# Performance work log

Measured on AMD Instinct MI355X. Metric: run time of the kernel, lower is better.

Reference implementation:

```python
import jax, jax.numpy as jnp
import numpy as np

N = 8192      # nodes
E = 262144    # edges (avg degree 32)
NFEAT = 1024
NHID = 512
ZDIM = 32


def _uniform(key, shape, stdv):
    return jax.random.uniform(key, shape, jnp.float32, -stdv, stdv)


def setup_inputs() -> dict:
    key = jax.random.key(0)
    ks = jax.random.split(key, 10)
    x = jax.random.normal(ks[0], (N, NFEAT), jnp.float32)
    adj_rows = jnp.sort(jax.random.randint(ks[1], (E,), 0, N))
    adj_cols = jax.random.randint(ks[2], (E,), 0, N)
    # positive edge weights, roughly row-normalized (avg degree 32)
    adj_vals = jax.random.uniform(ks[3], (E,), jnp.float32) / 32.0
    s0 = 1.0 / np.sqrt(NHID).astype(np.float32)
    s1 = 1.0 / np.sqrt(ZDIM).astype(np.float32)
    W0 = _uniform(ks[4], (NFEAT, NHID), s0)
    b0 = _uniform(ks[5], (NHID,), s0)
    W1 = _uniform(ks[6], (NHID, ZDIM), s1)
    b1 = _uniform(ks[7], (ZDIM,), s1)
    W2 = _uniform(ks[8], (NHID, ZDIM), s1)
    b2 = _uniform(ks[9], (ZDIM,), s1)
    return dict(x=x, adj_vals=adj_vals, W0=W0, b0=b0, W1=W1, b1=b1,
                W2=W2, b2=b2, adj_rows=adj_rows, adj_cols=adj_cols)


def _spmm(rows, cols, vals, mat):
    # sparse [N,N] @ dense [N,D] via gather + segment_sum
    return jax.ops.segment_sum(vals[:, None] * mat[cols], rows, num_segments=N)


def reference(x, adj_vals, W0, b0, W1, b1, W2, b2, adj_rows, adj_cols):
    # GraphConvolution: spmm(adj, x @ W) + b  (eval mode: dropout is identity)
    h = jax.nn.relu(_spmm(adj_rows, adj_cols, adj_vals, x @ W0) + b0)
    mu = jax.nn.relu(_spmm(adj_rows, adj_cols, adj_vals, h @ W1) + b1)
    logvar = jax.nn.relu(_spmm(adj_rows, adj_cols, adj_vals, h @ W2) + b2)
    z = mu  # reparameterize in eval mode returns mu
    adj_recon = jax.nn.sigmoid(z @ z.T)  # [N, N] inner-product decoder
    return adj_recon, z, mu, logvar
```

## Files before the change

### kernel.cpp

```cpp
#include <hip/hip_runtime.h>
#include <hip/hip_bf16.h>

typedef __bf16 bf16_t;
typedef __bf16 bf16x8 __attribute__((ext_vector_type(8)));
typedef float f32x4 __attribute__((ext_vector_type(4)));

#define NN 8192
#define EE 262144
#define NF 1024
#define NH 512
#define ZD 32

__global__ __launch_bounds__(256) void k_cvt(const float* __restrict__ in,
                                             bf16_t* __restrict__ out, int n8) {
  int i = blockIdx.x * 256 + threadIdx.x;
  if (i >= n8) return;
  const float4 a = ((const float4*)in)[i * 2];
  const float4 b = ((const float4*)in)[i * 2 + 1];
  bf16x8 o;
  o[0] = (bf16_t)a.x; o[1] = (bf16_t)a.y; o[2] = (bf16_t)a.z; o[3] = (bf16_t)a.w;
  o[4] = (bf16_t)b.x; o[5] = (bf16_t)b.y; o[6] = (bf16_t)b.z; o[7] = (bf16_t)b.w;
  ((bf16x8*)out)[i] = o;
}

__global__ __launch_bounds__(256) void k_transpose_cvt(const float* __restrict__ in,
                                                       bf16_t* __restrict__ out,
                                                       int R, int C) {
  __shared__ float tile[32][33];
  const int c0 = blockIdx.x * 32, r0 = blockIdx.y * 32;
  const int tx = threadIdx.x & 31, ty = threadIdx.x >> 5;
  #pragma unroll
  for (int i = ty; i < 32; i += 8)
    tile[i][tx] = in[(size_t)(r0 + i) * C + (c0 + tx)];
  __syncthreads();
  #pragma unroll
  for (int i = ty; i < 32; i += 8)
    out[(size_t)(c0 + i) * R + (r0 + tx)] = (bf16_t)tile[tx][i];
}

__global__ __launch_bounds__(256) void k_transpose_w12(const float* __restrict__ W1,
                                                       const float* __restrict__ W2,
                                                       bf16_t* __restrict__ out) {
  __shared__ float tile[32][33];
  const float* in = blockIdx.z ? W2 : W1;
  bf16_t* o = out + (size_t)blockIdx.z * ZD * NH;
  const int r0 = blockIdx.y * 32;
  const int tx = threadIdx.x & 31, ty = threadIdx.x >> 5;
  #pragma unroll
  for (int i = ty; i < 32; i += 8)
    tile[i][tx] = in[(size_t)(r0 + i) * ZD + tx];
  __syncthreads();
  #pragma unroll
  for (int i = ty; i < 32; i += 8)
    o[(size_t)(i)*NH + (r0 + tx)] = (bf16_t)tile[tx][i];
}

__global__ void k_rowptr(const int* __restrict__ rows, int* __restrict__ rp,
                         int n, int e) {
  int r = blockIdx.x * 256 + threadIdx.x;
  if (r > n) return;
  if (r == n) { rp[n] = e; return; }
  int lo = 0, hi = e;
  while (lo < hi) { int mid = (lo + hi) >> 1; if (rows[mid] < r) lo = mid + 1; else hi = mid; }
  rp[r] = lo;
}

__global__ __launch_bounds__(256) void k_gemm_bt_128x128(
    const bf16_t* __restrict__ A, const bf16_t* __restrict__ Bt,
    bf16_t* __restrict__ C, int M, int N, int K) {
  __shared__ bf16_t As[128 * 32];
  __shared__ bf16_t Bs[128 * 32];
  const int tid = threadIdx.x;
  const int lane = tid & 63, wave = tid >> 6;
  const int wx = wave & 1, wy = wave >> 1;
  const int m0 = blockIdx.y * 128, n0 = blockIdx.x * 128;
  const int q = lane >> 4, ml = lane & 15;

  const int sr = tid >> 2, ss = tid & 3;
  const int sw_lo = sr * 32 + ((ss ^ (sr & 3)) * 8);
  const int sw_hi = sw_lo + 64 * 32;

  int a_off[4], b_off[4];
  #pragma unroll
  for (int i = 0; i < 4; ++i) {
    int m = wy * 64 + i * 16 + ml;
    a_off[i] = m * 32 + ((q ^ (m & 3)) * 8);
    int n = wx * 64 + i * 16 + ml;
    b_off[i] = n * 32 + ((q ^ (n & 3)) * 8);
  }

  f32x4 acc[4][4];
  #pragma unroll
  for (int i = 0; i < 4; ++i)
    #pragma unroll
    for (int j = 0; j < 4; ++j)
      acc[i][j] = (f32x4){0.f, 0.f, 0.f, 0.f};

  const bf16_t* ga = A + (size_t)(m0 + sr) * K + ss * 8;
  const bf16_t* gb = Bt + (size_t)(n0 + sr) * K + ss * 8;
  const size_t stride64 = (size_t)64 * K;

  for (int k0 = 0; k0 < K; k0 += 32) {
    int4 va0 = *(const int4*)(ga + k0);
    int4 va1 = *(const int4*)(ga + stride64 + k0);
    int4 vb0 = *(const int4*)(gb + k0);
    int4 vb1 = *(const int4*)(gb + stride64 + k0);
    __syncthreads();
    *(int4*)(&As[sw_lo]) = va0;
    *(int4*)(&As[sw_hi]) = va1;
    *(int4*)(&Bs[sw_lo]) = vb0;
    *(int4*)(&Bs[sw_hi]) = vb1;
    __syncthreads();
    bf16x8 af[4], bfr[4];
    #pragma unroll
    for (int i = 0; i < 4; ++i) af[i] = *(const bf16x8*)(&As[a_off[i]]);
    #pragma unroll
    for (int j = 0; j < 4; ++j) bfr[j] = *(const bf16x8*)(&Bs[b_off[j]]);
    #pragma unroll
    for (int i = 0; i < 4; ++i)
      #pragma unroll
      for (int j = 0; j < 4; ++j)
        acc[i][j] = __builtin_amdgcn_mfma_f32_16x16x32_bf16(af[i], bfr[j], acc[i][j], 0, 0, 0);
  }

  #pragma unroll
  for (int i = 0; i < 4; ++i) {
    const int row = m0 + wy * 64 + i * 16 + q * 4;
    #pragma unroll
    for (int j = 0; j < 4; ++j) {
      const int col = n0 + wx * 64 + j * 16 + ml;
      #pragma unroll
      for (int r = 0; r < 4; ++r)
        C[(size_t)(row + r) * N + col] = (bf16_t)acc[i][j][r];
    }
  }
}

__global__ __launch_bounds__(256) void k_gemm_bt_128x64(
    const bf16_t* __restrict__ A, const bf16_t* __restrict__ Bt,
    float* __restrict__ C, int M, int N, int K) {
  __shared__ bf16_t As[128 * 32];
  __shared__ bf16_t Bs[64 * 32];
  const int tid = threadIdx.x;
  const int lane = tid & 63, wave = tid >> 6;
  const int m0 = blockIdx.y * 128;
  const int q = lane >> 4, ml = lane & 15;
  const int sr = tid >> 2, ss = tid & 3;
  const int sw_lo = sr * 32 + ((ss ^ (sr & 3)) * 8);
  const int sw_hi = sw_lo + 64 * 32;

  int a_off[2], b_off[4];
  #pragma unroll
  for (int i = 0; i < 2; ++i) {
    int m = wave * 32 + i * 16 + ml;
    a_off[i] = m * 32 + ((q ^ (m & 3)) * 8);
  }
  #pragma unroll
  for (int j = 0; j < 4; ++j) {
    int n = j * 16 + ml;
    b_off[j] = n * 32 + ((q ^ (n & 3)) * 8);
  }

  f32x4 acc[2][4];
  #pragma unroll
  for (int i = 0; i < 2; ++i)
    #pragma unroll
    for (int j = 0; j < 4; ++j)
      acc[i][j] = (f32x4){0.f, 0.f, 0.f, 0.f};

  const bf16_t* ga = A + (size_t)(m0 + sr) * K + ss * 8;
  const bf16_t* gb = Bt + (size_t)sr * K + ss * 8;
  const size_t stride64 = (size_t)64 * K;

  for (int k0 = 0; k0 < K; k0 += 32) {
    int4 va0 = *(const int4*)(ga + k0);
    int4 va1 = *(const int4*)(ga + stride64 + k0);
    int4 vb0 = *(const int4*)(gb + k0);
    __syncthreads();
    *(int4*)(&As[sw_lo]) = va0;
    *(int4*)(&As[sw_hi]) = va1;
    *(int4*)(&Bs[sw_lo]) = vb0;
    __syncthreads();
    bf16x8 af[2], bfr[4];
    #pragma unroll
    for (int i = 0; i < 2; ++i) af[i] = *(const bf16x8*)(&As[a_off[i]]);
    #pragma unroll
    for (int j = 0; j < 4; ++j) bfr[j] = *(const bf16x8*)(&Bs[b_off[j]]);
    #pragma unroll
    for (int i = 0; i < 2; ++i)
      #pragma unroll
      for (int j = 0; j < 4; ++j)
        acc[i][j] = __builtin_amdgcn_mfma_f32_16x16x32_bf16(af[i], bfr[j], acc[i][j], 0, 0, 0);
  }

  #pragma unroll
  for (int i = 0; i < 2; ++i) {
    const int row = m0 + wave * 32 + i * 16 + q * 4;
    #pragma unroll
    for (int j = 0; j < 4; ++j) {
      const int col = j * 16 + ml;
      #pragma unroll
      for (int r = 0; r < 4; ++r)
        C[(size_t)(row + r) * N + col] = acc[i][j][r];
    }
  }
}

__global__ __launch_bounds__(64) void k_spmm_h(
    const int* __restrict__ rp, const int* __restrict__ cols,
    const float* __restrict__ vals, const unsigned int* __restrict__ XW0b,
    const float* __restrict__ b0, bf16_t* __restrict__ h) {
  const int row = blockIdx.x >> 2, chunk = blockIdx.x & 3;
  const int t = threadIdx.x;
  const unsigned int* tab = XW0b + chunk * 64 + t;
  int e = rp[row];
  const int end = rp[row + 1];
  float a0 = 0.f, a1 = 0.f;
  for (; e + 1 < end; e += 2) {
    const int c0 = cols[e], c1 = cols[e + 1];
    const float v0 = vals[e], v1 = vals[e + 1];
    const unsigned int p0 = tab[(size_t)c0 * 256];
    const unsigned int p1 = tab[(size_t)c1 * 256];
    a0 += v0 * __uint_as_float(p0 << 16);
    a1 += v0 * __uint_as_float(p0 & 0xffff0000u);
    a0 += v1 * __uint_as_float(p1 << 16);
    a1 += v1 * __uint_as_float(p1 & 0xffff0000u);
  }
  if (e < end) {
    const float v0 = vals[e];
    const unsigned int p0 = tab[(size_t)cols[e] * 256];
    a0 += v0 * __uint_as_float(p0 << 16);
    a1 += v0 * __uint_as_float(p0 & 0xffff0000u);
  }
  const int d = chunk * 128 + t * 2;
  a0 += b0[d];
  a1 += b0[d + 1];
  bf16_t* o = h + (size_t)row * NH + d;
  o[0] = (bf16_t)fmaxf(a0, 0.f);
  o[1] = (bf16_t)fmaxf(a1, 0.f);
}

__global__ __launch_bounds__(64) void k_spmm_z(
    const int* __restrict__ rp, const int* __restrict__ cols,
    const float* __restrict__ vals, const float* __restrict__ HW,
    const float* __restrict__ b1, const float* __restrict__ b2,
    float* __restrict__ out_z, float* __restrict__ out_mu,
    float* __restrict__ out_lv, bf16_t* __restrict__ zb) {
  const int r = blockIdx.x;
  const int t = threadIdx.x;
  int e = rp[r];
  const int end = rp[r + 1];
  float acc = 0.f;
  for (; e + 1 < end; e += 2) {
    const float v0 = vals[e], v1 = vals[e + 1];
    const float s0 = HW[(size_t)cols[e] * 64 + t];
    const float s1 = HW[(size_t)cols[e + 1] * 64 + t];
    acc += v0 * s0 + v1 * s1;
  }
  if (e < end) acc += vals[e] * HW[(size_t)cols[e] * 64 + t];
  const float b = (t < ZD) ? b1[t] : b2[t - ZD];
  const float v = fmaxf(acc + b, 0.f);
  if (t < ZD) {
    out_mu[(size_t)r * ZD + t] = v;
    out_z[(size_t)r * ZD + t] = v;
    zb[(size_t)r * ZD + t] = (bf16_t)v;
  } else {
    out_lv[(size_t)r * ZD + (t - ZD)] = v;
  }
}

__global__ __launch_bounds__(256) void k_decoder(const bf16_t* __restrict__ Z,
                                                 float* __restrict__ out) {
  __shared__ bf16_t Zr[128 * 32];
  __shared__ bf16_t Zc[128 * 32];
  const int tid = threadIdx.x;
  const int lane = tid & 63, wave = tid >> 6;
  const int wx = wave & 1, wy = wave >> 1;
  const int m0 = blockIdx.y * 128, n0 = blockIdx.x * 128;
  const int q = lane >> 4, ml = lane & 15;
  const int sr = tid >> 2, ss = tid & 3;
  const int sw_lo = sr * 32 + ((ss ^ (sr & 3)) * 8);
  const int sw_hi = sw_lo + 64 * 32;

  *(int4*)(&Zr[sw_lo]) = *((const int4*)(Z + (size_t)(m0 + sr) * ZD) + ss);
  *(int4*)(&Zr[sw_hi]) = *((const int4*)(Z + (size_t)(m0 + sr + 64) * ZD) + ss);
  *(int4*)(&Zc[sw_lo]) = *((const int4*)(Z + (size_t)(n0 + sr) * ZD) + ss);
  *(int4*)(&Zc[sw_hi]) = *((const int4*)(Z + (size_t)(n0 + sr + 64) * ZD) + ss);
  __syncthreads();

  bf16x8 af[4], bfr[4];
  #pragma unroll
  for (int i = 0; i < 4; ++i) {
    int m = wy * 64 + i * 16 + ml;
    af[i] = *(const bf16x8*)(&Zr[m * 32 + ((q ^ (m & 3)) * 8)]);
    int n = wx * 64 + i * 16 + ml;
    bfr[i] = *(const bf16x8*)(&Zc[n * 32 + ((q ^ (n & 3)) * 8)]);
  }
  const f32x4 zero = (f32x4){0.f, 0.f, 0.f, 0.f};
  #pragma unroll
  for (int i = 0; i < 4; ++i) {
    const int row = m0 + wy * 64 + i * 16 + q * 4;
    #pragma unroll
    for (int j = 0; j < 4; ++j) {
      const int col = n0 + wx * 64 + j * 16 + ml;
      f32x4 c = __builtin_amdgcn_mfma_f32_16x16x32_bf16(af[i], bfr[j], zero, 0, 0, 0);
      #pragma unroll
      for (int r = 0; r < 4; ++r)
        out[(size_t)(row + r) * NN + col] = 1.f / (1.f + __expf(-c[r]));
    }
  }
}

extern "C" void kernel_launch(void* const* d_in, const int* in_sizes, int n_in,
                              void* d_out, int out_size, void* d_ws, size_t ws_size,
                              hipStream_t stream) {
  const float* x        = (const float*)d_in[0];
  const float* adj_vals = (const float*)d_in[1];
  const float* W0       = (const float*)d_in[2];
  const float* b0       = (const float*)d_in[3];
  const float* W1       = (const float*)d_in[4];
  const float* b1       = (const float*)d_in[5];
  const float* W2       = (const float*)d_in[6];
  const float* b2       = (const float*)d_in[7];
  const int* adj_rows   = (const int*)d_in[8];
  const int* adj_cols   = (const int*)d_in[9];

  char* ws = (char*)d_ws;
  bf16_t* XW0b = (bf16_t*)(ws);
  float*  HW   = (float*)(ws + 8388608);
  bf16_t* h    = (bf16_t*)(ws + 10485760);
  bf16_t* W0t  = (bf16_t*)(ws + 18874368);
  bf16_t* Wct  = (bf16_t*)(ws + 19922944);
  bf16_t* xb   = (bf16_t*)(ws + 19988480);
  bf16_t* zb   = (bf16_t*)(ws + 36765696);
  int*    rp   = (int*)(ws + 37289984);

  float* out     = (float*)d_out;
  float* out_adj = out;
  float* out_z   = out + (size_t)NN * NN;
  float* out_mu  = out_z + (size_t)NN * ZD;
  float* out_lv  = out_mu + (size_t)NN * ZD;

  k_cvt<<<(NN * NF / 8 + 255) / 256, 256, 0, stream>>>(x, xb, NN * NF / 8);
  k_transpose_cvt<<<dim3(NH / 32, NF / 32), 256, 0, stream>>>(W0, W0t, NF, NH);
  k_transpose_w12<<<dim3(1, NH / 32, 2), 256, 0, stream>>>(W1, W2, Wct);
  k_rowptr<<<33, 256, 0, stream>>>(adj_rows, rp, NN, EE);

  k_gemm_bt_128x128<<<dim3(NH / 128, NN / 128), 256, 0, stream>>>(xb, W0t, XW0b, NN, NH, NF);
  k_spmm_h<<<NN * 4, 64, 0, stream>>>(rp, adj_cols, adj_vals,
                                      (const unsigned int*)XW0b, b0, h);

  k_gemm_bt_128x64<<<dim3(1, NN / 128), 256, 0, stream>>>(h, Wct, HW, NN, 64, NH);
  k_spmm_z<<<NN, 64, 0, stream>>>(rp, adj_cols, adj_vals, HW, b1, b2, out_z, out_mu, out_lv, zb);

  k_decoder<<<dim3(NN / 128, NN / 128), 256, 0, stream>>>(zb, out_adj);
}
```

Before: 434.7 us.

## Stage decoder output through LDS for coalesced nontemporal stores; batch SpMM rows per block

The decoder now computes all sigmoid tiles in registers, stages each 64x128 half-tile in shared memory, and writes full rows with 16-byte nontemporal stores instead of scattered 4-byte stores. This targets write coalescing on the 256MB output, which dominates runtime, at the cost of extra LDS use and two barriers per half. Both SpMM kernels move from 64-thread to 256-thread blocks handling four rows each and unroll the edge loop by four. k_spmm_h also packs its two bf16 outputs into one 32-bit store.

```diff
diff --git a/kernel.cpp b/kernel.cpp
--- a/kernel.cpp
+++ b/kernel.cpp
@@ -206,27 +206,34 @@
   }
 }
 
-__global__ __launch_bounds__(64) void k_spmm_h(
+__global__ __launch_bounds__(256) void k_spmm_h(
     const int* __restrict__ rp, const int* __restrict__ cols,
     const float* __restrict__ vals, const unsigned int* __restrict__ XW0b,
     const float* __restrict__ b0, bf16_t* __restrict__ h) {
-  const int row = blockIdx.x >> 2, chunk = blockIdx.x & 3;
-  const int t = threadIdx.x;
+  const int chunk = blockIdx.x & 3;
+  const int row = (blockIdx.x >> 2) * 4 + (threadIdx.x >> 6);
+  const int t = threadIdx.x & 63;
   const unsigned int* tab = XW0b + chunk * 64 + t;
   int e = rp[row];
   const int end = rp[row + 1];
   float a0 = 0.f, a1 = 0.f;
-  for (; e + 1 < end; e += 2) {
-    const int c0 = cols[e], c1 = cols[e + 1];
-    const float v0 = vals[e], v1 = vals[e + 1];
+  for (; e + 3 < end; e += 4) {
+    const int c0 = cols[e], c1 = cols[e + 1], c2 = cols[e + 2], c3 = cols[e + 3];
+    const float v0 = vals[e], v1 = vals[e + 1], v2 = vals[e + 2], v3 = vals[e + 3];
     const unsigned int p0 = tab[(size_t)c0 * 256];
     const unsigned int p1 = tab[(size_t)c1 * 256];
+    const unsigned int p2 = tab[(size_t)c2 * 256];
+    const unsigned int p3 = tab[(size_t)c3 * 256];
     a0 += v0 * __uint_as_float(p0 << 16);
     a1 += v0 * __uint_as_float(p0 & 0xffff0000u);
     a0 += v1 * __uint_as_float(p1 << 16);
     a1 += v1 * __uint_as_float(p1 & 0xffff0000u);
-  }
-  if (e < end) {
+    a0 += v2 * __uint_as_float(p2 << 16);
+    a1 += v2 * __uint_as_float(p2 & 0xffff0000u);
+    a0 += v3 * __uint_as_float(p3 << 16);
+    a1 += v3 * __uint_as_float(p3 & 0xffff0000u);
+  }
+  for (; e < end; ++e) {
     const float v0 = vals[e];
     const unsigned int p0 = tab[(size_t)cols[e] * 256];
     a0 += v0 * __uint_as_float(p0 << 16);
@@ -235,29 +242,36 @@
   const int d = chunk * 128 + t * 2;
   a0 += b0[d];
   a1 += b0[d + 1];
-  bf16_t* o = h + (size_t)row * NH + d;
-  o[0] = (bf16_t)fmaxf(a0, 0.f);
-  o[1] = (bf16_t)fmaxf(a1, 0.f);
-}
-
-__global__ __launch_bounds__(64) void k_spmm_z(
+  bf16_t x0 = (bf16_t)fmaxf(a0, 0.f);
+  bf16_t x1 = (bf16_t)fmaxf(a1, 0.f);
+  const unsigned int pk = (unsigned int)(*(const unsigned short*)&x0) |
+                          ((unsigned int)(*(const unsigned short*)&x1) << 16);
+  *(unsigned int*)(h + (size_t)row * NH + d) = pk;
+}
+
+__global__ __launch_bounds__(256) void k_spmm_z(
     const int* __restrict__ rp, const int* __restrict__ cols,
     const float* __restrict__ vals, const float* __restrict__ HW,
     const float* __restrict__ b1, const float* __restrict__ b2,
     float* __restrict__ out_z, float* __restrict__ out_mu,
     float* __restrict__ out_lv, bf16_t* __restrict__ zb) {
-  const int r = blockIdx.x;
-  const int t = threadIdx.x;
+  const int r = blockIdx.x * 4 + (threadIdx.x >> 6);
+  const int t = threadIdx.x & 63;
   int e = rp[r];
   const int end = rp[r + 1];
   float acc = 0.f;
-  for (; e + 1 < end; e += 2) {
-    const float v0 = vals[e], v1 = vals[e + 1];
+  for (; e + 3 < end; e += 4) {
+    const float v0 = vals[e], v1 = vals[e + 1], v2 = vals[e + 2], v3 = vals[e + 3];
     const float s0 = HW[(size_t)cols[e] * 64 + t];
     const float s1 = HW[(size_t)cols[e + 1] * 64 + t];
-    acc += v0 * s0 + v1 * s1;
-  }
-  if (e < end) acc += vals[e] * HW[(size_t)cols[e] * 64 + t];
+    const float s2 = HW[(size_t)cols[e + 2] * 64 + t];
+    const float s3 = HW[(size_t)cols[e + 3] * 64 + t];
+    acc += v0 * s0;
+    acc += v1 * s1;
+    acc += v2 * s2;
+    acc += v3 * s3;
+  }
+  for (; e < end; ++e) acc += vals[e] * HW[(size_t)cols[e] * 64 + t];
   const float b = (t < ZD) ? b1[t] : b2[t - ZD];
   const float v = fmaxf(acc + b, 0.f);
   if (t < ZD) {
@@ -273,6 +287,7 @@
                                                  float* __restrict__ out) {
   __shared__ bf16_t Zr[128 * 32];
   __shared__ bf16_t Zc[128 * 32];
+  __shared__ float tile[64][132];
   const int tid = threadIdx.x;
   const int lane = tid & 63, wave = tid >> 6;
   const int wx = wave & 1, wy = wave >> 1;
@@ -296,18 +311,44 @@
     int n = wx * 64 + i * 16 + ml;
     bfr[i] = *(const bf16x8*)(&Zc[n * 32 + ((q ^ (n & 3)) * 8)]);
   }
+
+  f32x4 acc[4][4];
   const f32x4 zero = (f32x4){0.f, 0.f, 0.f, 0.f};
   #pragma unroll
-  for (int i = 0; i < 4; ++i) {
-    const int row = m0 + wy * 64 + i * 16 + q * 4;
-    #pragma unroll
-    for (int j = 0; j < 4; ++j) {
-      const int col = n0 + wx * 64 + j * 16 + ml;
-      f32x4 c = __builtin_amdgcn_mfma_f32_16x16x32_bf16(af[i], bfr[j], zero, 0, 0, 0);
+  for (int i = 0; i < 4; ++i)
+    #pragma unroll
+    for (int j = 0; j < 4; ++j)
+      acc[i][j] = __builtin_amdgcn_mfma_f32_16x16x32_bf16(af[i], bfr[j], zero, 0, 0, 0);
+
+  #pragma unroll
+  for (int i = 0; i < 4; ++i)
+    #pragma unroll
+    for (int j = 0; j < 4; ++j)
       #pragma unroll
       for (int r = 0; r < 4; ++r)
-        out[(size_t)(row + r) * NN + col] = 1.f / (1.f + __expf(-c[r]));
+        acc[i][j][r] = 1.f / (1.f + __expf(-acc[i][j][r]));
+
+  const int g = tid >> 5, c4 = tid & 31;
+  #pragma unroll
+  for (int half = 0; half < 2; ++half) {
+    if (wy == half) {
+      #pragma unroll
+      for (int i = 0; i < 4; ++i)
+        #pragma unroll
+        for (int j = 0; j < 4; ++j)
+          #pragma unroll
+          for (int r = 0; r < 4; ++r)
+            tile[i * 16 + q * 4 + r][wx * 64 + j * 16 + ml] = acc[i][j][r];
     }
+    __syncthreads();
+    float* orow = out + (size_t)(m0 + half * 64) * NN + n0;
+    #pragma unroll
+    for (int p = 0; p < 8; ++p) {
+      const int lr = p * 8 + g;
+      f32x4 v = *(const f32x4*)&tile[lr][c4 * 4];
+      __builtin_nontemporal_store(v, (f32x4*)(orow + (size_t)lr * NN + c4 * 4));
+    }
+    __syncthreads();
   }
 }
 
@@ -347,11 +388,11 @@
   k_rowptr<<<33, 256, 0, stream>>>(adj_rows, rp, NN, EE);
 
   k_gemm_bt_128x128<<<dim3(NH / 128, NN / 128), 256, 0, stream>>>(xb, W0t, XW0b, NN, NH, NF);
-  k_spmm_h<<<NN * 4, 64, 0, stream>>>(rp, adj_cols, adj_vals,
-                                      (const unsigned int*)XW0b, b0, h);
+  k_spmm_h<<<NN, 256, 0, stream>>>(rp, adj_cols, adj_vals,
+                                   (const unsigned int*)XW0b, b0, h);
 
   k_gemm_bt_128x64<<<dim3(1, NN / 128), 256, 0, stream>>>(h, Wct, HW, NN, 64, NH);
-  k_spmm_z<<<NN, 64, 0, stream>>>(rp, adj_cols, adj_vals, HW, b1, b2, out_z, out_mu, out_lv, zb);
+  k_spmm_z<<<NN / 4, 256, 0, stream>>>(rp, adj_cols, adj_vals, HW, b1, b2, out_z, out_mu, out_lv, zb);
 
   k_decoder<<<dim3(NN / 128, NN / 128), 256, 0, stream>>>(zb, out_adj);
 }
```

Result: faster. 399.7 us (-8.0%).
